# Performance work log

Measured on AMD Instinct MI355X. Metric: run time of the kernel, lower is better.

Reference implementation:

```python
import jax, jax.numpy as jnp
import numpy as np

P1, P2 = 24, 168          # period1 (daily), period2 (weekly)
MAX_H = 336               # max(hs)
BS, N, F = 64, 512, 16


def mult_seasindex(y, p):
    # average each phase over the first two full cycles, normalize by the mean
    bs, n, f = y.shape
    avg = y[:, :2 * p, :].reshape(bs, 2, p, f).mean(axis=1)          # (bs, p, f)
    return avg / y[:, :2 * p, :].mean(axis=1, keepdims=True)


def mult_init_params(y):
    bs, n, f = y.shape
    I1 = mult_seasindex(y, P1)                                        # (bs, P1, f)
    w1 = mult_seasindex(y, P2) / jnp.tile(I1, (1, P2 // P1, 1))       # (bs, P2, f)
    x = jnp.concatenate([jnp.zeros((bs, 1, f), y.dtype),
                         jnp.diff(y[:, :P2, :], axis=1)], axis=1)
    t = jnp.mean((y[:, :P2, :] - y[:, P2:2 * P2, :]) / P2 + x, axis=1) / 2
    s = jnp.mean(y[:, :2 * P2, :], axis=1) - (P2 + 0.5) * t
    return I1, w1, t, s


def reference(y, alphas, betas, gammas, omegas, phis):
    bs, n, f = y.shape
    a = jax.nn.sigmoid(alphas)
    b = jax.nn.sigmoid(betas)
    g = jax.nn.sigmoid(gammas)
    o = jax.nn.sigmoid(omegas)

    Ic, wc, t, s = mult_init_params(y)

    idx1 = jnp.arange(n) % P1
    idx2 = jnp.arange(n) % P2
    ys = jnp.transpose(y, (1, 0, 2))                                  # (n, bs, f)

    def step(carry, inp):
        Ic, wc, s, t = carry
        yt, i1, i2 = inp
        Icv = jax.lax.dynamic_slice_in_dim(Ic, i1, 1, axis=1)[:, 0, :]
        wcv = jax.lax.dynamic_slice_in_dim(wc, i2, 1, axis=1)[:, 0, :]
        yhat_t = (s + t) * Icv * wcv
        snew = a * (yt / (Icv * wcv)) + (1 - a) * (s + t)
        tnew = b * (snew - s) + (1 - b) * t
        Icn = jax.lax.dynamic_update_slice_in_dim(
            Ic, (g * (yt / (snew * wcv)) + (1 - g) * Icv)[:, None, :], i1, axis=1)
        wcn = jax.lax.dynamic_update_slice_in_dim(
            wc, (o * (yt / (snew * Icv)) + (1 - o) * wcv)[:, None, :], i2, axis=1)
        return (Icn, wcn, snew, tnew), yhat_t

    (Ic, wc, s, t), yhat = jax.lax.scan(step, (Ic, wc, s, t), (ys, idx1, idx2))
    yhat = jnp.transpose(yhat, (1, 0, 2))                             # (bs, n, f)

    Ic = jnp.roll(Ic, (-n) % P1, axis=1)
    wc = jnp.roll(wc, (-n) % P2, axis=1)
    e = y - yhat

    # forecast horizon (multiplicative, enable_ar=False)
    h = jnp.arange(1, MAX_H + 1, dtype=y.dtype)
    ca = s[:, None, :] + h[None, :, None] * t[:, None, :]             # (bs, MAX_H, f)
    cb = jnp.tile(Ic, (1, MAX_H // P1 + 1, 1))[:, :MAX_H, :]
    cc = jnp.tile(wc, (1, MAX_H // P2 + 1, 1))[:, :MAX_H, :]
    fcast = ca * cb * cc
    return fcast, yhat, e, Ic, wc, t, s


def setup_inputs() -> dict:
    key = jax.random.key(0)
    k0, k1, k2, k3, k4, k5 = jax.random.split(key, 6)
    y = jax.random.uniform(k0, (BS, N, F), jnp.float32, minval=5.0, maxval=15.0)
    p = lambda k: 0.001 + 0.01 * jax.random.normal(k, (F,), jnp.float32)
    return {"y": y, "alphas": p(k1), "betas": p(k2), "gammas": p(k3),
            "omegas": p(k4), "phis": p(k5)}
```

## Files before the change

### kernel.cpp

```cpp
#include <hip/hip_runtime.h>
#include <math.h>


#define P1c   24
#define P2c   168
#define NSTEP 512
#define BSc   64
#define NFc   16
#define MAXH  336
#define NSERIES 1024

#define OFF_FC   0
#define OFF_YH   (BSc * MAXH * NFc)
#define OFF_E    (OFF_YH + BSc * NSTEP * NFc)
#define OFF_IC   (OFF_E  + BSc * NSTEP * NFc)
#define OFF_WC   (OFF_IC + BSc * P1c * NFc)
#define OFF_T    (OFF_WC + BSc * P2c * NFc)
#define OFF_S    (OFF_T  + BSc * NFc)

__device__ __forceinline__ double nrcp(double a) {
    double x = __builtin_amdgcn_rcp(a);
    x = fma(fma(-a, x, 1.0), x, x);
    x = fma(fma(-a, x, 1.0), x, x);
    return x;
}

__device__ __forceinline__ double nrcp1(double a) {
    double x = __builtin_amdgcn_rcp(a);
    x = fma(fma(-a, x, 1.0), x, x);
    return x;
}

template<int I>
__device__ __forceinline__ double bcast8(double v) {
    constexpr int pat = (I << 5) | 0x18;
    int lo = __builtin_amdgcn_ds_swizzle(__double2loint(v), pat);
    int hi = __builtin_amdgcn_ds_swizzle(__double2hiint(v), pat);
    return __hiloint2double(hi, lo);
}
template<int M>
__device__ __forceinline__ double xor8(double v) {
    constexpr int pat = (M << 10) | 0x1f;
    int lo = __builtin_amdgcn_ds_swizzle(__double2loint(v), pat);
    int hi = __builtin_amdgcn_ds_swizzle(__double2hiint(v), pat);
    return __hiloint2double(hi, lo);
}

__global__ __launch_bounds__(128, 1)
void dshw_one(const float* __restrict__ y,
              const float* __restrict__ alphas,
              const float* __restrict__ betas,
              const float* __restrict__ gammas,
              const float* __restrict__ omegas,
              float* __restrict__ out)
{
    __shared__ double sW[P2c][NFc];
    __shared__ double sIc[P1c][NFc];
    __shared__ __align__(16) float sY[NSTEP][NFc];

    const int tid   = threadIdx.x;
    const int s_loc = tid >> 3;
    const int j     = tid & 7;
    const int bb    = blockIdx.x;
    const int f     = s_loc;

    const float4* __restrict__ y4 =
        (const float4*)(y + (size_t)bb * NSTEP * NFc);
    #pragma unroll 4
    for (int i = tid; i < (NSTEP * NFc) / 4; i += 128) {
        float4 v = y4[i];
        *(float4*)&sY[i >> 2][(i & 3) * 4] = v;
    }
    __syncthreads();

    const double al = 1.0 / (1.0 + exp(-(double)alphas[f]));
    const double be = 1.0 / (1.0 + exp(-(double)betas[f]));
    const double ga = 1.0 / (1.0 + exp(-(double)gammas[f]));
    const double om = 1.0 / (1.0 + exp(-(double)omegas[f]));
    const double one_m_al = 1.0 - al, one_m_be = 1.0 - be;
    const double one_p_be = 1.0 + be;
    const double one_m_ga = 1.0 - ga, one_m_om = 1.0 - om;
    const double inv_al = nrcp(al);
    const double ga_al  = ga * inv_al;
    const double om_al  = om * inv_al;
    const double A_ = one_p_be * one_m_al + one_m_be;

    double Pl = (j == 0) ? 1.0 : 0.0;
    double Ql = 0.0;
    {
        double p = 1.0, q = 0.0, pn = 0.0, qn = 1.0;
        #pragma unroll
        for (int it = 1; it <= 7; ++it) {
            double p2 = fma(A_, p, -pn);
            double q2 = fma(A_, q, -qn);
            pn = one_m_al * p; qn = one_m_al * q;
            p = p2; q = q2;
            if (j == it) { Pl = p; Ql = q; }
        }
    }
    double R_[8];
    R_[0] = one_p_be;
    {
        double r = one_p_be, rn = 1.0;
        #pragma unroll
        for (int m = 1; m < 8; ++m) {
            double r2 = fma(A_, r, -rn);
            rn = one_m_al * r;
            r = r2;
            R_[m] = r;
        }
    }
    double cf[8];
    #pragma unroll
    for (int i = 0; i < 8; ++i) cf[i] = 0.0;
    #pragma unroll
    for (int i = 0; i < 7; ++i) {
        #pragma unroll
        for (int m = 0; m + i + 1 <= 7; ++m) {
            if (j == i + m + 1) cf[i] = R_[m];
        }
    }

    double pa = 0.0, pb = 0.0;
    #pragma unroll
    for (int m = 0; m < 21; ++m) {
        pa += (double)sY[j + 8 * m][s_loc];
        pb += (double)sY[j + 8 * m + P2c][s_loc];
    }
    pa += xor8<1>(pa); pb += xor8<1>(pb);
    pa += xor8<2>(pa); pb += xor8<2>(pb);
    pa += xor8<4>(pa); pb += xor8<4>(pb);
    const double sa = pa, sb = pb;

    double Icr_own[3];
    {
        double icv[3];
        double pc = 0.0;
        #pragma unroll
        for (int m2 = 0; m2 < 3; ++m2) {
            const int ph = j + 8 * m2;
            double v0 = (double)sY[ph][s_loc];
            double v1 = (double)sY[ph + P1c][s_loc];
            icv[m2] = 0.5 * (v0 + v1);
            pc += v0 + v1;
        }
        pc += xor8<1>(pc);
        pc += xor8<2>(pc);
        pc += xor8<4>(pc);
        const double inv_mean48 = 48.0 * nrcp(pc);
        #pragma unroll
        for (int m2 = 0; m2 < 3; ++m2) Icr_own[m2] = icv[m2] * inv_mean48;
    }

    const double mean336     = (sa + sb) * (1.0 / 336.0);
    const double inv_mean336 = nrcp(mean336);
    {
        double rI[3];
        #pragma unroll
        for (int m2 = 0; m2 < 3; ++m2)
            rI[m2] = inv_mean336 * nrcp(Icr_own[m2]);
        #pragma unroll
        for (int m = 0; m < 21; ++m) {
            const int row = j + 8 * m;
            double v0 = (double)sY[row][s_loc];
            double v1 = (double)sY[row + P2c][s_loc];
            sW[row][s_loc] = 0.5 * (v0 + v1) * rI[m % 3];
        }
    }

    double tt0 = 0.5 * ((sa - sb) * (1.0 / (168.0 * 168.0)) +
                        ((double)sY[P2c - 1][s_loc] - (double)sY[0][s_loc]) * (1.0 / 168.0));
    double ss0 = mean336 - 168.5 * tt0;

    double spt0 = ss0 + tt0;
    double snp0 = ss0;

    double xPrev = 0.0, wcPrev = 0.0;
    int wrow = 0, prow = 0, Kb = 0;

#define WIN8(SEL, PSEL, HASD)                                                 \
    {                                                                         \
        double wcv = sW[wrow + j][s_loc];                                     \
        double yv  = (double)sY[Kb + j][s_loc];                               \
        if (HASD) {                                                           \
            Icr_own[PSEL] *= fma(ga_al, xPrev, one_m_ga);                     \
            sW[prow + j][s_loc] = wcPrev * fma(om_al, xPrev, one_m_om);       \
        }                                                                     \
        double iw  = Icr_own[SEL] * wcv;                                      \
        double inv = nrcp1(iw);                                               \
        double aur = (al * yv) * inv;                                         \
        double acc = fma(Pl, spt0, Ql * snp0);                                \
        acc = fma(cf[0], bcast8<0>(aur), acc);                                \
        acc = fma(cf[1], bcast8<1>(aur), acc);                                \
        acc = fma(cf[2], bcast8<2>(aur), acc);                                \
        acc = fma(cf[3], bcast8<3>(aur), acc);                                \
        acc = fma(cf[4], bcast8<4>(aur), acc);                                \
        acc = fma(cf[5], bcast8<5>(aur), acc);                                \
        acc = fma(cf[6], bcast8<6>(aur), acc);                                \
        acc = fma(cf[7], bcast8<7>(aur), acc);                                \
        double s6b = bcast8<6>(acc);                                          \
        double s7b = bcast8<7>(acc);                                          \
        double a6b = bcast8<6>(aur);                                          \
        double a7b = bcast8<7>(aur);                                          \
        double yhat = acc * iw;                                               \
        sY[Kb + j][s_loc] = (float)yhat;                                      \
        double snw = fma(one_m_al, acc, aur);                                 \
        xPrev  = aur * __builtin_amdgcn_rcp(snw);                             \
        wcPrev = wcv;                                                         \
        double snew7 = fma(one_m_al, s7b, a7b);                               \
        double snew6 = fma(one_m_al, s6b, a6b);                               \
        spt0 = fma(one_p_be, snew7, fma(one_m_be, s7b, -snew6));              \
        snp0 = snew7;                                                         \
        prow = wrow;                                                          \
        wrow = (wrow + 8 == P2c) ? 0 : wrow + 8;                              \
        Kb += 8;                                                              \
    }

    WIN8(0, 0, false)
    WIN8(1, 0, true)
    WIN8(2, 1, true)
    for (int k = 0; k < 20; ++k) {
        WIN8(0, 2, true)
        WIN8(1, 0, true)
        WIN8(2, 1, true)
    }
    WIN8(0, 2, true)
#undef WIN8

    Icr_own[0] *= fma(ga_al, xPrev, one_m_ga);
    sW[prow + j][s_loc] = wcPrev * fma(om_al, xPrev, one_m_om);

    const double ss_f = snp0;
    const double tt_f = spt0 - snp0;

    sIc[j     ][s_loc] = Icr_own[0];
    sIc[j + 8 ][s_loc] = Icr_own[1];
    sIc[j + 16][s_loc] = Icr_own[2];

    {
        float* __restrict__ ic_o = out + OFF_IC + (size_t)bb * P1c * NFc + f;
        ic_o[((j + 16) % P1c) * NFc] = (float)Icr_own[0];
        ic_o[( j            ) * NFc] = (float)Icr_own[1];
        ic_o[((j + 8 ) % P1c) * NFc] = (float)Icr_own[2];
    }
    {
        float* __restrict__ wc_o = out + OFF_WC + (size_t)bb * P2c * NFc + f;
        #pragma unroll
        for (int m = 0; m < 21; ++m) {
            const int row = j + 8 * m;
            const int jj  = (row >= 8) ? (row - 8) : (row + 160);
            wc_o[jj * NFc] = (float)sW[row][s_loc];
        }
    }
    if (j == 0) {
        out[OFF_T + bb * NFc + f] = (float)tt_f;
        out[OFF_S + bb * NFc + f] = (float)ss_f;
    }

    __syncthreads();
    {
        float* __restrict__ yho = out + OFF_YH + (size_t)bb * NSTEP * NFc;
        float* __restrict__ eo  = out + OFF_E  + (size_t)bb * NSTEP * NFc;
        #pragma unroll 4
        for (int i = tid; i < (NSTEP * NFc) / 4; i += 128) {
            float4 yh4 = *(const float4*)&sY[i >> 2][(i & 3) * 4];
            float4 yv4 = y4[i];
            ((float4*)yho)[i] = yh4;
            float4 ev;
            ev.x = yv4.x - yh4.x; ev.y = yv4.y - yh4.y;
            ev.z = yv4.z - yh4.z; ev.w = yv4.w - yh4.w;
            ((float4*)eo)[i] = ev;
        }
    }
    __syncthreads();

    {
        int p1i = j + 8;
        int p2i = j + 8;
        #pragma unroll 6
        for (int m = 0; m < 42; ++m) {
            const int k = j + 8 * m;
            double cb = sIc[p1i][s_loc];
            double cc = sW[p2i][s_loc];
            double ca = fma((double)(k + 1), tt_f, ss_f);
            sY[k][s_loc] = (float)(ca * cb * cc);
            p1i += 8; p1i = (p1i >= P1c) ? (p1i - P1c) : p1i;
            p2i += 8; p2i = (p2i >= P2c) ? (p2i - P2c) : p2i;
        }
    }
    __syncthreads();

    {
        float* __restrict__ fco = out + OFF_FC + (size_t)bb * MAXH * NFc;
        #pragma unroll 4
        for (int i = tid; i < (MAXH * NFc) / 4; i += 128) {
            ((float4*)fco)[i] = *(const float4*)&sY[i >> 2][(i & 3) * 4];
        }
    }
}

extern "C" void kernel_launch(void* const* d_in, const int* in_sizes, int n_in,
                              void* d_out, int out_size, void* d_ws, size_t ws_size,
                              hipStream_t stream)
{
    const float* y      = (const float*)d_in[0];
    const float* alphas = (const float*)d_in[1];
    const float* betas  = (const float*)d_in[2];
    const float* gammas = (const float*)d_in[3];
    const float* omegas = (const float*)d_in[4];
    float* out = (float*)d_out;

    hipLaunchKernelGGL(dshw_one, dim3(BSc), dim3(128), 0, stream,
                       y, alphas, betas, gammas, omegas, out);
}
```

Measured before the change: 83.14 us.

## Software-pipeline the 8-step recurrence window and stage Wc output through shared memory

The serial loop over 8-step windows is split into a prefetch stage (load the next window, reciprocal, broadcast the aur values), a deferred update of the previous window's seasonal indices, and a shorter serial critical path. The serial path now uses a tree-reduced dot product and reads the boundary values from snew directly. This takes the loads and reciprocals off the window-to-window dependency chain, at the cost of more live registers. Separately, the Wc output is now staged in shared memory after the forecast rows and written with coalesced float4 stores instead of scattered scalar global writes.

```diff
diff --git a/kernel.cpp b/kernel.cpp
--- a/kernel.cpp
+++ b/kernel.cpp
@@ -175,60 +175,82 @@
     double spt0 = ss0 + tt0;
     double snp0 = ss0;
 
-    double xPrev = 0.0, wcPrev = 0.0;
-    int wrow = 0, prow = 0, Kb = 0;
-
-#define WIN8(SEL, PSEL, HASD)                                                 \
+    double b0, b1, b2, b3, b4, b5, b6, b7;
+    double n0, n1, n2, n3, n4, n5, n6, n7;
+    double aurC, aurN, aurP;
+    double iwC, iwN;
+    double wcC, wcN, wcP;
+    double snwP = 0.0;
+    int rowC, rowN, rowP, KbC, KbN;
+
+#define PRE(SEL)                                                              \
     {                                                                         \
-        double wcv = sW[wrow + j][s_loc];                                     \
-        double yv  = (double)sY[Kb + j][s_loc];                               \
-        if (HASD) {                                                           \
-            Icr_own[PSEL] *= fma(ga_al, xPrev, one_m_ga);                     \
-            sW[prow + j][s_loc] = wcPrev * fma(om_al, xPrev, one_m_om);       \
-        }                                                                     \
-        double iw  = Icr_own[SEL] * wcv;                                      \
-        double inv = nrcp1(iw);                                               \
-        double aur = (al * yv) * inv;                                         \
-        double acc = fma(Pl, spt0, Ql * snp0);                                \
-        acc = fma(cf[0], bcast8<0>(aur), acc);                                \
-        acc = fma(cf[1], bcast8<1>(aur), acc);                                \
-        acc = fma(cf[2], bcast8<2>(aur), acc);                                \
-        acc = fma(cf[3], bcast8<3>(aur), acc);                                \
-        acc = fma(cf[4], bcast8<4>(aur), acc);                                \
-        acc = fma(cf[5], bcast8<5>(aur), acc);                                \
-        acc = fma(cf[6], bcast8<6>(aur), acc);                                \
-        acc = fma(cf[7], bcast8<7>(aur), acc);                                \
-        double s6b = bcast8<6>(acc);                                          \
-        double s7b = bcast8<7>(acc);                                          \
-        double a6b = bcast8<6>(aur);                                          \
-        double a7b = bcast8<7>(aur);                                          \
-        double yhat = acc * iw;                                               \
-        sY[Kb + j][s_loc] = (float)yhat;                                      \
-        double snw = fma(one_m_al, acc, aur);                                 \
-        xPrev  = aur * __builtin_amdgcn_rcp(snw);                             \
-        wcPrev = wcv;                                                         \
-        double snew7 = fma(one_m_al, s7b, a7b);                               \
-        double snew6 = fma(one_m_al, s6b, a6b);                               \
-        spt0 = fma(one_p_be, snew7, fma(one_m_be, s7b, -snew6));              \
-        snp0 = snew7;                                                         \
-        prow = wrow;                                                          \
-        wrow = (wrow + 8 == P2c) ? 0 : wrow + 8;                              \
-        Kb += 8;                                                              \
-    }
-
-    WIN8(0, 0, false)
-    WIN8(1, 0, true)
-    WIN8(2, 1, true)
-    for (int k = 0; k < 20; ++k) {
-        WIN8(0, 2, true)
-        WIN8(1, 0, true)
-        WIN8(2, 1, true)
-    }
-    WIN8(0, 2, true)
-#undef WIN8
-
-    Icr_own[0] *= fma(ga_al, xPrev, one_m_ga);
-    sW[prow + j][s_loc] = wcPrev * fma(om_al, xPrev, one_m_om);
+        wcN = sW[rowN + j][s_loc];                                            \
+        double yvN = (double)sY[KbN + j][s_loc];                              \
+        iwN = Icr_own[SEL] * wcN;                                             \
+        double invN = nrcp1(iwN);                                             \
+        aurN = (al * yvN) * invN;                                             \
+        n0 = bcast8<0>(aurN); n1 = bcast8<1>(aurN);                           \
+        n2 = bcast8<2>(aurN); n3 = bcast8<3>(aurN);                           \
+        n4 = bcast8<4>(aurN); n5 = bcast8<5>(aurN);                           \
+        n6 = bcast8<6>(aurN); n7 = bcast8<7>(aurN);                           \
+    }
+#define DPR(PSEL)                                                             \
+    {                                                                         \
+        double x = aurP * __builtin_amdgcn_rcp(snwP);                         \
+        Icr_own[PSEL] *= fma(ga_al, x, one_m_ga);                             \
+        sW[rowP + j][s_loc] = wcP * fma(om_al, x, one_m_om);                  \
+    }
+#define SER                                                                   \
+    double snwS;                                                              \
+    {                                                                         \
+        double t0 = fma(cf[0], b0, cf[1] * b1);                               \
+        double t1 = fma(cf[2], b2, cf[3] * b3);                               \
+        double t2 = fma(cf[4], b4, cf[5] * b5);                               \
+        double t3 = fma(cf[6], b6, cf[7] * b7);                               \
+        double v  = (t0 + t1) + (t2 + t3);                                    \
+        double acc = fma(Pl, spt0, fma(Ql, snp0, v));                         \
+        snwS = fma(one_m_al, acc, aurC);                                      \
+        sY[KbC + j][s_loc] = (float)(acc * iwC);                              \
+        double accB7 = bcast8<7>(acc);                                        \
+        double snwB7 = bcast8<7>(snwS);                                       \
+        double snwB6 = bcast8<6>(snwS);                                       \
+        spt0 = fma(one_p_be, snwB7, fma(one_m_be, accB7, -snwB6));            \
+        snp0 = snwB7;                                                         \
+    }
+#define ROT                                                                   \
+    {                                                                         \
+        aurP = aurC; snwP = snwS; wcP = wcC; rowP = rowC;                     \
+        aurC = aurN; iwC = iwN; wcC = wcN;                                    \
+        b0 = n0; b1 = n1; b2 = n2; b3 = n3;                                   \
+        b4 = n4; b5 = n5; b6 = n6; b7 = n7;                                   \
+        rowC = rowN; rowN = (rowN + 8 == P2c) ? 0 : rowN + 8;                 \
+        KbC = KbN; KbN += 8;                                                  \
+    }
+
+    rowN = 0; KbN = 0;
+    PRE(0)
+    b0 = n0; b1 = n1; b2 = n2; b3 = n3; b4 = n4; b5 = n5; b6 = n6; b7 = n7;
+    aurC = aurN; iwC = iwN; wcC = wcN;
+    rowC = 0; KbC = 0; rowP = 0; wcP = 0.0; aurP = 0.0;
+    rowN = 8; KbN = 8;
+
+    { PRE(1) SER ROT }
+    { PRE(2) DPR(0) SER ROT }
+    { PRE(0) DPR(1) SER ROT }
+    #pragma unroll 1
+    for (int it = 0; it < 20; ++it) {
+        { PRE(1) DPR(2) SER ROT }
+        { PRE(2) DPR(0) SER ROT }
+        { PRE(0) DPR(1) SER ROT }
+    }
+    { DPR(2) SER ROT }
+    DPR(0)
+
+#undef PRE
+#undef DPR
+#undef SER
+#undef ROT
 
     const double ss_f = snp0;
     const double tt_f = spt0 - snp0;
@@ -242,15 +264,6 @@
         ic_o[((j + 16) % P1c) * NFc] = (float)Icr_own[0];
         ic_o[( j            ) * NFc] = (float)Icr_own[1];
         ic_o[((j + 8 ) % P1c) * NFc] = (float)Icr_own[2];
-    }
-    {
-        float* __restrict__ wc_o = out + OFF_WC + (size_t)bb * P2c * NFc + f;
-        #pragma unroll
-        for (int m = 0; m < 21; ++m) {
-            const int row = j + 8 * m;
-            const int jj  = (row >= 8) ? (row - 8) : (row + 160);
-            wc_o[jj * NFc] = (float)sW[row][s_loc];
-        }
     }
     if (j == 0) {
         out[OFF_T + bb * NFc + f] = (float)tt_f;
@@ -287,6 +300,12 @@
             p1i += 8; p1i = (p1i >= P1c) ? (p1i - P1c) : p1i;
             p2i += 8; p2i = (p2i >= P2c) ? (p2i - P2c) : p2i;
         }
+        #pragma unroll
+        for (int m = 0; m < 21; ++m) {
+            const int row = j + 8 * m;
+            const int jj  = (row >= 8) ? (row - 8) : (row + 160);
+            sY[MAXH + jj][s_loc] = (float)sW[row][s_loc];
+        }
     }
     __syncthreads();
 
@@ -295,6 +314,11 @@
         #pragma unroll 4
         for (int i = tid; i < (MAXH * NFc) / 4; i += 128) {
             ((float4*)fco)[i] = *(const float4*)&sY[i >> 2][(i & 3) * 4];
+        }
+        float* __restrict__ wco = out + OFF_WC + (size_t)bb * P2c * NFc;
+        #pragma unroll 4
+        for (int i = tid; i < (P2c * NFc) / 4; i += 128) {
+            ((float4*)wco)[i] = *(const float4*)&sY[MAXH + (i >> 2)][(i & 3) * 4];
         }
     }
 }
```

After: 83.82 us. About the same (+0.8%).
